# Optimization experiments

Measured on AMD Instinct MI355X. Metric: run time of the kernel, lower is better.

The kernel has to match this reference:

```python
import jax, jax.numpy as jnp
import numpy as np

B, FEAT, H, W = 16, 64, 32, 32


def setup_inputs() -> dict:
    key = jax.random.key(0)
    ks = jax.random.split(key, 8)
    s = 0.05
    return {
        "x": jax.random.normal(ks[0], (B, 2 * FEAT, H, W), jnp.float32),
        # i2s_conv: MaskConv(2F -> 4F, 1x1, maskB with group=1 == all-ones), bias=False
        "w_i2s": jax.random.normal(ks[1], (4 * FEAT, 2 * FEAT), jnp.float32) * s,
        # left/right state-to-state Conv2d(F -> 4F, kernel (2,1)), with bias
        "w_left": jax.random.normal(ks[2], (4 * FEAT, FEAT, 2), jnp.float32) * s,
        "b_left": jax.random.normal(ks[3], (4 * FEAT,), jnp.float32) * s,
        "w_right": jax.random.normal(ks[4], (4 * FEAT, FEAT, 2), jnp.float32) * s,
        "b_right": jax.random.normal(ks[5], (4 * FEAT,), jnp.float32) * s,
        # skip_conv: MaskConv(F -> 2F, 1x1, maskB group=1 == plain conv), bias=True
        "w_skip": jax.random.normal(ks[6], (2 * FEAT, FEAT), jnp.float32) * s,
        "b_skip": jax.random.normal(ks[7], (2 * FEAT,), jnp.float32) * s,
    }


def _shift_right_w(a):  # F.pad(a,(1,0,...))[..., :-1]
    return jnp.pad(a, ((0, 0), (0, 0), (0, 0), (1, 0)))[:, :, :, :-1]


def _shift_left_w(a):  # F.pad(a,(0,1,...))[..., 1:]
    return jnp.pad(a, ((0, 0), (0, 0), (0, 0), (0, 1)))[:, :, :, 1:]


def _shift_down_h(a):  # pad one row on top, drop last row
    return jnp.pad(a, ((0, 0), (0, 0), (1, 0), (0, 0)))[:, :, :-1, :]


def _s2s(hprev, w, b, wshift):
    # pad(top=1, side=1) + Conv2d kernel (2,1) + crop one column, expressed as
    # two 1x1 contractions on width-shifted / (width+height)-shifted maps.
    hw = wshift(hprev)            # [B,F,H,W] shifted one column
    hd = _shift_down_h(hw)        # additionally shifted one row down
    return (jnp.einsum('bchw,oc->bohw', hd, w[:, :, 0])
            + jnp.einsum('bchw,oc->bohw', hw, w[:, :, 1])
            + b[None, :, None, None])


def _forward(x, w_i2s, w_left, b_left, w_right, b_right, w_skip, b_skip):
    b_, c2, h_, w_ = x.shape
    f = c2 // 2
    hmap = jnp.einsum('bchw,oc->bohw', x, w_i2s)  # [B,4F,H,W]
    left_h = hmap   # stew: input-to-state shared between directions
    right_h = hmap
    zeros = jnp.zeros((b_, f, h_, w_), x.dtype)

    def step(carry, _):
        lc, lh, rc, rh = carry
        pre = jax.nn.sigmoid(_s2s(lh, w_left, b_left, _shift_right_w) + left_h)
        o, fg, ig, g = jnp.split(pre, 4, axis=1)
        lc = fg * lc + ig * g
        lh = o * jnp.tanh(lc)
        pre = jax.nn.sigmoid(_s2s(rh, w_right, b_right, _shift_left_w) + right_h)
        o, fg, ig, g = jnp.split(pre, 4, axis=1)
        rc = fg * rc + ig * g
        rh = o * jnp.tanh(rc)
        return (lc, lh, rc, rh), None

    (lc, lh, rc, rh), _ = jax.lax.scan(step, (zeros, zeros, zeros, zeros), None, length=h_)
    rh = _shift_down_h(rh)  # unstew + shift right stream down one row
    out_h = lh + rh         # [B,F,H,W]
    skip = jnp.einsum('bchw,oc->bohw', out_h, w_skip) + b_skip[None, :, None, None]
    return x + skip


def reference(x, w_i2s, w_left, b_left, w_right, b_right, w_skip, b_skip):
    return _forward(x, w_i2s, w_left, b_left, w_right, b_right, w_skip, b_skip)
```

## Files before the change

### kernel.cpp

```cpp
#include <hip/hip_runtime.h>


using bf16   = __bf16;
using bf16x8 = __attribute__((ext_vector_type(8))) __bf16;
using f32x4  = __attribute__((ext_vector_type(4))) float;

#define SCOPE_AGENT __HIP_MEMORY_SCOPE_AGENT
#define LOG2E 1.4426950408889634f
#define K2E   2.8853900817779268f

__device__ __forceinline__ bf16x8 bzero8() {
  bf16x8 v;
#pragma unroll
  for (int e = 0; e < 8; ++e) v[e] = (bf16)0.0f;
  return v;
}
__device__ __forceinline__ unsigned short f2bu(float f) {
  bf16 b = (bf16)f;
  return __builtin_bit_cast(unsigned short, b);
}
__device__ __forceinline__ float bu2f(unsigned short u) {
  return __uint_as_float(((unsigned)u) << 16);
}
__device__ __forceinline__ float dw_lo(unsigned u) { return __uint_as_float(u << 16); }
__device__ __forceinline__ float dw_hi(unsigned u) { return __uint_as_float(u & 0xffff0000u); }

__global__ void prep_kernel(const float* __restrict__ w_i2s,
                            const float* __restrict__ w_left,
                            const float* __restrict__ w_right,
                            const float* __restrict__ w_skip,
                            bf16* __restrict__ WnI, bf16* __restrict__ WnL,
                            bf16* __restrict__ WnR, bf16* __restrict__ WnS) {
  int t = blockIdx.x * 256 + threadIdx.x;
  if (t < 32768) {
    WnI[t] = (bf16)w_i2s[t];
    int o = t >> 7, k = t & 127;
    int src = (k < 64) ? (o * 128 + k * 2) : (o * 128 + (k - 64) * 2 + 1);
    WnL[t] = (bf16)(w_left[src] * LOG2E);
    WnR[t] = (bf16)(w_right[src] * LOG2E);
    if (t < 8192) WnS[t] = (bf16)w_skip[t];
  }
}

__global__ __launch_bounds__(256, 2)
void hmap_kernel(const float* __restrict__ x, const bf16* __restrict__ Wn,
                 const float* __restrict__ bL, const float* __restrict__ bR,
                 ushort4* __restrict__ hmapL, ushort4* __restrict__ hmapR) {
  __shared__ __align__(16) bf16 At[64 * 128];
  const int tile = blockIdx.x;
  const int b = tile >> 4, h0 = (tile & 15) << 1;
  const int t = threadIdx.x;
  const float* xb = x + (size_t)(b * 128) * 1024 + h0 * 32;
#pragma unroll
  for (int i = 0; i < 8; ++i) {
    int idx = t + 256 * i;
    int cc = idx >> 4, m4 = idx & 15;
    f32x4 v = *(const f32x4*)(xb + (size_t)cc * 1024 + m4 * 4);
#pragma unroll
    for (int e = 0; e < 4; ++e) {
      int m = m4 * 4 + e;
      int kb = (cc * 2) ^ ((m & 7) << 4);
      *(bf16*)((char*)At + m * 256 + kb) = (bf16)v[e];
    }
  }
  __syncthreads();
  const int wv = t >> 6, l = t & 63;
  const int l15 = l & 15, lq = l >> 4;
  const int c = wv * 16 + l15;
  bf16x8 bfrag[4][4];
#pragma unroll
  for (int g = 0; g < 4; ++g)
#pragma unroll
    for (int kk = 0; kk < 4; ++kk)
      bfrag[g][kk] = *(const bf16x8*)(Wn + (g * 64 + c) * 128 + kk * 32 + lq * 8);
  float blq[4], brq[4];
#pragma unroll
  for (int g = 0; g < 4; ++g) {
    blq[g] = bL[g * 64 + c] * LOG2E;
    brq[g] = bR[g * 64 + c] * LOG2E;
  }
  f32x4 acc[4][4];
  const f32x4 fz = {0.f, 0.f, 0.f, 0.f};
#pragma unroll
  for (int ms = 0; ms < 4; ++ms)
#pragma unroll
    for (int g = 0; g < 4; ++g) acc[ms][g] = fz;
#pragma unroll
  for (int kk = 0; kk < 4; ++kk) {
#pragma unroll
    for (int ms = 0; ms < 4; ++ms) {
      int m = ms * 16 + l15;
      int kb = ((kk * 32 + lq * 8) * 2) ^ ((m & 7) << 4);
      bf16x8 a = *(const bf16x8*)((const char*)At + m * 256 + kb);
#pragma unroll
      for (int g = 0; g < 4; ++g)
        acc[ms][g] =
            __builtin_amdgcn_mfma_f32_16x16x32_bf16(a, bfrag[g][kk], acc[ms][g], 0, 0, 0);
    }
  }
  const int pix0 = tile * 64;
#pragma unroll
  for (int ms = 0; ms < 4; ++ms)
#pragma unroll
    for (int j = 0; j < 4; ++j) {
      int p = pix0 + ms * 16 + lq * 4 + j;
      ushort4 hl, hr;
      float a0 = acc[ms][0][j] * LOG2E, a1 = acc[ms][1][j] * LOG2E;
      float a2 = acc[ms][2][j] * LOG2E, a3 = acc[ms][3][j] * LOG2E;
      hl.x = f2bu(a0 + blq[0]); hl.y = f2bu(a1 + blq[1]);
      hl.z = f2bu(a2 + blq[2]); hl.w = f2bu(a3 + blq[3]);
      hr.x = f2bu(a0 + brq[0]); hr.y = f2bu(a1 + brq[1]);
      hr.z = f2bu(a2 + brq[2]); hr.w = f2bu(a3 + brq[3]);
      hmapL[(size_t)p * 64 + c] = hl;
      hmapR[(size_t)p * 64 + c] = hr;
    }
}

__global__ __launch_bounds__(512, 4)
void scan_kernel(bf16* __restrict__ lhLout, bf16* __restrict__ lhRout,
                 const ushort4* __restrict__ hmapL,
                 const ushort4* __restrict__ hmapR,
                 const bf16* __restrict__ WnL, const bf16* __restrict__ WnR,
                 bf16* __restrict__ ring, unsigned* __restrict__ prodFlag,
                 unsigned* __restrict__ consFlag) {
  __shared__ __align__(16) bf16 buf[2][3 * 32 * 64];
  __shared__ __align__(16) ushort4 hlds[64 * 65];
  const int blk = blockIdx.x;
  const int q = blk & 31, tl = blk >> 5;
  const bool right = (q & 1) != 0;
  const int b = q >> 1;
  const int r0 = tl * 2;
  const int t = threadIdx.x;
  const int dw = right ? 1 : -1;
  bf16* __restrict__ lout = right ? lhRout : lhLout;
  const bf16* __restrict__ Wn = right ? WnR : WnL;
  const ushort4* __restrict__ hsrc =
      (right ? hmapR : hmapL) + (size_t)(b * 1024 + r0 * 32) * 64;
  const int w8 = t >> 6, l = t & 63, l15 = l & 15, lq = l >> 4;
  const int wv = w8 & 3, mhalf = w8 >> 2;
  const int c = wv * 16 + l15;
  const int wb_ = mhalf * 16;

#pragma unroll
  for (int i = 0; i < 8; ++i) {
    int idx = t + 512 * i;
    int px = idx >> 6, cc = idx & 63;
    hlds[px * 65 + cc] = hsrc[idx];
  }
#pragma unroll
  for (int i = 0; i < 2; ++i) {
    int idx = t + 512 * i;
    if (idx < 768) ((bf16x8*)buf[0])[idx] = bzero8();
  }
  if (t < 256) ((bf16x8*)buf[1])[t] = bzero8();

  bf16x8 bfrag[4][4];
#pragma unroll
  for (int g = 0; g < 4; ++g)
#pragma unroll
    for (int kk = 0; kk < 4; ++kk)
      bfrag[g][kk] = *(const bf16x8*)(Wn + (g * 64 + c) * 128 + kk * 32 + lq * 8);
  float lcA[4], lcB[4];
#pragma unroll
  for (int j = 0; j < 4; ++j) {
    lcA[j] = 0.0f;
    lcB[j] = 0.0f;
  }

  const unsigned* pBelow = prodFlag + (size_t)(blk - 32) * 32;
  const unsigned* cAbove = consFlag + (size_t)(blk + 32) * 32;
  unsigned* myProd = prodFlag + (size_t)blk * 32;
  unsigned* myCons = consFlag + (size_t)blk * 32;

  const int wsrc = wb_ + l15 + dw;
  const bool oob = (unsigned)wsrc >= 32u;
  const int wc = wsrc & 31;
  const int swz = (wc & 7) << 4;

  __syncthreads();

#pragma unroll 1
  for (int s = 0; s < 32; ++s) {
    bf16* curb = buf[s & 1];
    bf16* nxtb = buf[(s + 1) & 1];
    const bool consume = (tl > 0) && (s > 0);
    const bool publish = (tl < 15) && (s < 31);
    bf16* slotOut = ring + (size_t)(((s & 3) * 512) + blk) * 2048;

    if (consume) {
      const unsigned tgt = (unsigned)s;
      while (__hip_atomic_load(pBelow, __ATOMIC_RELAXED, SCOPE_AGENT) < tgt)
        __builtin_amdgcn_s_sleep(1);
      const bf16* slotIn =
          ring + (size_t)((((s - 1) & 3) * 512) + (blk - 32)) * 2048;
      int w = t >> 4, c4 = t & 15;
      const unsigned long long* src =
          (const unsigned long long*)(slotIn + w * 64 + c4 * 8);
      unsigned long long d0 = __hip_atomic_load(src, __ATOMIC_RELAXED, SCOPE_AGENT);
      int off = (w * 128 + c4 * 16) ^ ((w & 7) << 4);
      *(unsigned long long*)((char*)curb + off) = d0;
      int w2 = 0;
      (void)w2;
    }
    if (publish && s >= 4) {
      const unsigned tgt = (unsigned)(s - 3);
      while (__hip_atomic_load(cAbove, __ATOMIC_RELAXED, SCOPE_AGENT) < tgt)
        __builtin_amdgcn_s_sleep(1);
    }

    {
      f32x4 acc[4];
#pragma unroll
      for (int j2 = 0; j2 < 2; ++j2) {
        int w0 = wb_ + lq * 4 + j2 * 2;
        ushort4 h0 = hlds[(32 + w0) * 65 + c];
        ushort4 h1 = hlds[(32 + w0 + 1) * 65 + c];
        acc[0][j2 * 2] = bu2f(h0.x); acc[0][j2 * 2 + 1] = bu2f(h1.x);
        acc[1][j2 * 2] = bu2f(h0.y); acc[1][j2 * 2 + 1] = bu2f(h1.y);
        acc[2][j2 * 2] = bu2f(h0.z); acc[2][j2 * 2 + 1] = bu2f(h1.z);
        acc[3][j2 * 2] = bu2f(h0.w); acc[3][j2 * 2 + 1] = bu2f(h1.w);
      }
#pragma unroll
      for (int kk = 0; kk < 4; ++kk) {
        const int srcr = 1 + (kk >> 1);
        const int c0 = (kk & 1) * 32 + lq * 8;
        int aoff = ((srcr * 32 + wc) * 128 + c0 * 2) ^ swz;
        bf16x8 a = *(const bf16x8*)((const char*)curb + aoff);
        if (oob) a = bzero8();
#pragma unroll
        for (int g = 0; g < 4; ++g)
          acc[g] = __builtin_amdgcn_mfma_f32_16x16x32_bf16(a, bfrag[g][kk], acc[g], 0, 0, 0);
      }
#pragma unroll
      for (int j = 0; j < 4; ++j) {
        const int w = wb_ + lq * 4 + j;
        float e0 = __builtin_amdgcn_exp2f(-acc[0][j]);
        float e1 = __builtin_amdgcn_exp2f(-acc[1][j]);
        float e2 = __builtin_amdgcn_exp2f(-acc[2][j]);
        float e3 = __builtin_amdgcn_exp2f(-acc[3][j]);
        float fg = __builtin_amdgcn_rcpf(1.0f + e1);
        float igg = __builtin_amdgcn_rcpf((1.0f + e2) * (1.0f + e3));
        float lcv = fg * lcA[j] + K2E * igg;
        lcA[j] = lcv;
        float ey = __builtin_amdgcn_exp2f(-lcv);
        float lh = (1.0f - ey) * __builtin_amdgcn_rcpf((1.0f + e0) * (1.0f + ey));
        bf16 vb = (bf16)lh;
        int woff = ((2 * 32 + w) * 128 + c * 2) ^ ((w & 7) << 4);
        *(bf16*)((char*)nxtb + woff) = vb;
        if (publish) {
          unsigned u = (unsigned)__builtin_bit_cast(unsigned short, vb);
          unsigned pv = (unsigned)__shfl_xor((int)u, 1);
          if ((l & 1) == 0) {
            unsigned dword = u | (pv << 16);
            __hip_atomic_store((unsigned*)(slotOut + w * 64 + (c & ~1)), dword,
                               __ATOMIC_RELAXED, SCOPE_AGENT);
          }
        }
      }
    }
    __syncthreads();
    if (publish && t == 0)
      __hip_atomic_store(myProd, (unsigned)(s + 1), __ATOMIC_RELAXED, SCOPE_AGENT);
    if (consume && t == 64)
      __hip_atomic_store(myCons, (unsigned)s, __ATOMIC_RELAXED, SCOPE_AGENT);

    {
      f32x4 acc[4];
#pragma unroll
      for (int j2 = 0; j2 < 2; ++j2) {
        int w0 = wb_ + lq * 4 + j2 * 2;
        ushort4 h0 = hlds[w0 * 65 + c];
        ushort4 h1 = hlds[(w0 + 1) * 65 + c];
        acc[0][j2 * 2] = bu2f(h0.x); acc[0][j2 * 2 + 1] = bu2f(h1.x);
        acc[1][j2 * 2] = bu2f(h0.y); acc[1][j2 * 2 + 1] = bu2f(h1.y);
        acc[2][j2 * 2] = bu2f(h0.z); acc[2][j2 * 2 + 1] = bu2f(h1.z);
        acc[3][j2 * 2] = bu2f(h0.w); acc[3][j2 * 2 + 1] = bu2f(h1.w);
      }
#pragma unroll
      for (int kk = 0; kk < 4; ++kk) {
        const int srcr = kk >> 1;
        const int c0 = (kk & 1) * 32 + lq * 8;
        int aoff = ((srcr * 32 + wc) * 128 + c0 * 2) ^ swz;
        bf16x8 a = *(const bf16x8*)((const char*)curb + aoff);
        if (oob) a = bzero8();
#pragma unroll
        for (int g = 0; g < 4; ++g)
          acc[g] = __builtin_amdgcn_mfma_f32_16x16x32_bf16(a, bfrag[g][kk], acc[g], 0, 0, 0);
      }
#pragma unroll
      for (int j = 0; j < 4; ++j) {
        const int w = wb_ + lq * 4 + j;
        float e0 = __builtin_amdgcn_exp2f(-acc[0][j]);
        float e1 = __builtin_amdgcn_exp2f(-acc[1][j]);
        float e2 = __builtin_amdgcn_exp2f(-acc[2][j]);
        float e3 = __builtin_amdgcn_exp2f(-acc[3][j]);
        float fg = __builtin_amdgcn_rcpf(1.0f + e1);
        float igg = __builtin_amdgcn_rcpf((1.0f + e2) * (1.0f + e3));
        float lcv = fg * lcB[j] + K2E * igg;
        lcB[j] = lcv;
        float ey = __builtin_amdgcn_exp2f(-lcv);
        float lh = (1.0f - ey) * __builtin_amdgcn_rcpf((1.0f + e0) * (1.0f + ey));
        int woff = ((1 * 32 + w) * 128 + c * 2) ^ ((w & 7) << 4);
        *(bf16*)((char*)nxtb + woff) = (bf16)lh;
      }
    }
    __syncthreads();
  }

  {
    int R = 1 + (t >> 8), rem = t & 255;
    int w = rem >> 3, c8 = rem & 7;
    int off = ((R * 32 + w) * 128 + c8 * 16) ^ ((w & 7) << 4);
    bf16x8 v = *(const bf16x8*)((const char*)buf[0] + off);
    *(bf16x8*)(lout + (size_t)((b * 32 + r0 + R - 1) * 32 + w) * 64 + c8 * 8) = v;
  }
}

__global__ __launch_bounds__(256, 2)
void final_kernel(const float* __restrict__ x, const bf16* __restrict__ lhL,
                  const bf16* __restrict__ lhR, const bf16* __restrict__ Wn,
                  const float* __restrict__ b_skip, float* __restrict__ out) {
  __shared__ __align__(16) bf16 At[64 * 64];
  __shared__ __align__(16) float smemT[128 * 72];
  const int tile = blockIdx.x;
  const int b = tile >> 4, h0 = (tile & 15) << 1;
  const int t = threadIdx.x;
#pragma unroll
  for (int i = 0; i < 2; ++i) {
    int idx = t + 256 * i;
    int m = idx >> 3, c8 = idx & 7;
    int h = h0 + (m >> 5), w = m & 31;
    size_t p = (size_t)(b * 32 + h) * 32 + w;
    bf16x8 vL = *(const bf16x8*)(lhL + p * 64 + c8 * 8);
    bf16x8 v;
    if (h > 0) {
      bf16x8 vR = *(const bf16x8*)(lhR + (p - 32) * 64 + c8 * 8);
#pragma unroll
      for (int e = 0; e < 8; ++e) v[e] = (bf16)((float)vL[e] + (float)vR[e]);
    } else {
      v = vL;
    }
    int kb = (c8 * 16) ^ ((m & 7) << 4);
    *(bf16x8*)((char*)At + m * 128 + kb) = v;
  }
  __syncthreads();
  const int wv = t >> 6, l = t & 63;
  const int l15 = l & 15, lq = l >> 4;
  const int c = wv * 16 + l15;
  bf16x8 bfrag[2][2];
#pragma unroll
  for (int g = 0; g < 2; ++g)
#pragma unroll
    for (int kk = 0; kk < 2; ++kk)
      bfrag[g][kk] = *(const bf16x8*)(Wn + (g * 64 + c) * 64 + kk * 32 + lq * 8);
  f32x4 acc[4][2];
  const f32x4 fz = {0.f, 0.f, 0.f, 0.f};
#pragma unroll
  for (int ms = 0; ms < 4; ++ms)
#pragma unroll
    for (int g = 0; g < 2; ++g) acc[ms][g] = fz;
#pragma unroll
  for (int kk = 0; kk < 2; ++kk) {
#pragma unroll
    for (int ms = 0; ms < 4; ++ms) {
      int m = ms * 16 + l15;
      int kb = ((kk * 32 + lq * 8) * 2) ^ ((m & 7) << 4);
      bf16x8 a = *(const bf16x8*)((const char*)At + m * 128 + kb);
#pragma unroll
      for (int g = 0; g < 2; ++g)
        acc[ms][g] =
            __builtin_amdgcn_mfma_f32_16x16x32_bf16(a, bfrag[g][kk], acc[ms][g], 0, 0, 0);
    }
  }
  float bsk[2];
#pragma unroll
  for (int g = 0; g < 2; ++g) bsk[g] = b_skip[g * 64 + c];
#pragma unroll
  for (int ms = 0; ms < 4; ++ms)
#pragma unroll
    for (int g = 0; g < 2; ++g)
#pragma unroll
      for (int j = 0; j < 4; ++j) {
        int m = ms * 16 + lq * 4 + j;
        int n = g * 64 + c;
        smemT[n * 72 + m] = acc[ms][g][j] + bsk[g];
      }
  __syncthreads();
  const float* xb = x + (size_t)(b * 128) * 1024 + h0 * 32;
  float* ob = out + (size_t)(b * 128) * 1024 + h0 * 32;
#pragma unroll
  for (int i = 0; i < 8; ++i) {
    int idx = t + 256 * i;
    int o2 = idx >> 4, m4 = idx & 15;
    f32x4 s = *(const f32x4*)(&smemT[o2 * 72 + m4 * 4]);
    f32x4 xv = *(const f32x4*)(xb + (size_t)o2 * 1024 + m4 * 4);
#pragma unroll
    for (int e = 0; e < 4; ++e) s[e] += xv[e];
    *(f32x4*)(ob + (size_t)o2 * 1024 + m4 * 4) = s;
  }
}

extern "C" void kernel_launch(void* const* d_in, const int* in_sizes, int n_in,
                              void* d_out, int out_size, void* d_ws, size_t ws_size,
                              hipStream_t stream) {
  const float* x       = (const float*)d_in[0];
  const float* w_i2s   = (const float*)d_in[1];
  const float* w_left  = (const float*)d_in[2];
  const float* b_left  = (const float*)d_in[3];
  const float* w_right = (const float*)d_in[4];
  const float* b_right = (const float*)d_in[5];
  const float* w_skip  = (const float*)d_in[6];
  const float* b_skip  = (const float*)d_in[7];
  float* out = (float*)d_out;
  char* ws = (char*)d_ws;

  bf16*     lhL   = (bf16*)(ws + 0x0000000);
  bf16*     lhR   = (bf16*)(ws + 0x0200000);
  ushort4*  hmapL = (ushort4*)(ws + 0x0400000);
  ushort4*  hmapR = (ushort4*)(ws + 0x0C00000);
  bf16*     ring  = (bf16*)(ws + 0x1400000);
  unsigned* prodF = (unsigned*)(ws + 0x1C00000);
  unsigned* consF = (unsigned*)(ws + 0x1C10000);
  bf16*     WnI   = (bf16*)(ws + 0x1C20000);
  bf16*     WnL   = (bf16*)(ws + 0x1C30000);
  bf16*     WnR   = (bf16*)(ws + 0x1C40000);
  bf16*     WnS   = (bf16*)(ws + 0x1C50000);

  hipMemsetAsync(ws + 0x1C00000, 0, 0x20000, stream);
  prep_kernel<<<128, 256, 0, stream>>>(w_i2s, w_left, w_right, w_skip, WnI, WnL, WnR, WnS);
  hmap_kernel<<<256, 256, 0, stream>>>(x, WnI, b_left, b_right, hmapL, hmapR);
  scan_kernel<<<512, 512, 0, stream>>>(lhL, lhR, hmapL, hmapR, WnL, WnR,
                                       ring, prodF, consF);
  final_kernel<<<256, 256, 0, stream>>>(x, lhL, lhR, WnS, b_skip, out);
}
```

Before: 174.0 us.

## Feed ring halo rows straight into MFMA registers and drop mid-step barrier

The scan kernel no longer stages the halo row received from the block below into shared memory. Each lane now loads its MFMA A-fragments for that row directly from the global ring buffer into registers. This shrinks the LDS ping-pong buffer from three rows to two and removes one __syncthreads per step. The producer and consumer flag stores move to the end-of-step barrier, which may delay the publish signal to neighbouring blocks by half a step.

```diff
diff --git a/kernel.cpp b/kernel.cpp
--- a/kernel.cpp
+++ b/kernel.cpp
@@ -4,6 +4,7 @@
 using bf16   = __bf16;
 using bf16x8 = __attribute__((ext_vector_type(8))) __bf16;
 using f32x4  = __attribute__((ext_vector_type(4))) float;
+using u64x2  = __attribute__((ext_vector_type(2))) unsigned long long;
 
 #define SCOPE_AGENT __HIP_MEMORY_SCOPE_AGENT
 #define LOG2E 1.4426950408889634f
@@ -22,8 +23,6 @@
 __device__ __forceinline__ float bu2f(unsigned short u) {
   return __uint_as_float(((unsigned)u) << 16);
 }
-__device__ __forceinline__ float dw_lo(unsigned u) { return __uint_as_float(u << 16); }
-__device__ __forceinline__ float dw_hi(unsigned u) { return __uint_as_float(u & 0xffff0000u); }
 
 __global__ void prep_kernel(const float* __restrict__ w_i2s,
                             const float* __restrict__ w_left,
@@ -123,7 +122,7 @@
                  const bf16* __restrict__ WnL, const bf16* __restrict__ WnR,
                  bf16* __restrict__ ring, unsigned* __restrict__ prodFlag,
                  unsigned* __restrict__ consFlag) {
-  __shared__ __align__(16) bf16 buf[2][3 * 32 * 64];
+  __shared__ __align__(16) bf16 buf[2][2 * 32 * 64];
   __shared__ __align__(16) ushort4 hlds[64 * 65];
   const int blk = blockIdx.x;
   const int q = blk & 31, tl = blk >> 5;
@@ -147,12 +146,7 @@
     int px = idx >> 6, cc = idx & 63;
     hlds[px * 65 + cc] = hsrc[idx];
   }
-#pragma unroll
-  for (int i = 0; i < 2; ++i) {
-    int idx = t + 512 * i;
-    if (idx < 768) ((bf16x8*)buf[0])[idx] = bzero8();
-  }
-  if (t < 256) ((bf16x8*)buf[1])[t] = bzero8();
+  ((bf16x8*)buf[0])[t] = bzero8();
 
   bf16x8 bfrag[4][4];
 #pragma unroll
@@ -160,11 +154,11 @@
 #pragma unroll
     for (int kk = 0; kk < 4; ++kk)
       bfrag[g][kk] = *(const bf16x8*)(Wn + (g * 64 + c) * 128 + kk * 32 + lq * 8);
-  float lcA[4], lcB[4];
+  float lc0[4], lc1[4];
 #pragma unroll
   for (int j = 0; j < 4; ++j) {
-    lcA[j] = 0.0f;
-    lcB[j] = 0.0f;
+    lc0[j] = 0.0f;
+    lc1[j] = 0.0f;
   }
 
   const unsigned* pBelow = prodFlag + (size_t)(blk - 32) * 32;
@@ -187,20 +181,22 @@
     const bool publish = (tl < 15) && (s < 31);
     bf16* slotOut = ring + (size_t)(((s & 3) * 512) + blk) * 2048;
 
+    bf16x8 a_ring0 = bzero8(), a_ring1 = bzero8();
     if (consume) {
       const unsigned tgt = (unsigned)s;
       while (__hip_atomic_load(pBelow, __ATOMIC_RELAXED, SCOPE_AGENT) < tgt)
         __builtin_amdgcn_s_sleep(1);
-      const bf16* slotIn =
-          ring + (size_t)((((s - 1) & 3) * 512) + (blk - 32)) * 2048;
-      int w = t >> 4, c4 = t & 15;
-      const unsigned long long* src =
-          (const unsigned long long*)(slotIn + w * 64 + c4 * 8);
-      unsigned long long d0 = __hip_atomic_load(src, __ATOMIC_RELAXED, SCOPE_AGENT);
-      int off = (w * 128 + c4 * 16) ^ ((w & 7) << 4);
-      *(unsigned long long*)((char*)curb + off) = d0;
-      int w2 = 0;
-      (void)w2;
+      if (!oob) {
+        const unsigned long long* slotIn = (const unsigned long long*)(
+            ring + (size_t)((((s - 1) & 3) * 512) + (blk - 32)) * 2048 + wc * 64);
+        u64x2 v0, v1;
+        v0[0] = __hip_atomic_load(slotIn + lq * 2, __ATOMIC_RELAXED, SCOPE_AGENT);
+        v0[1] = __hip_atomic_load(slotIn + lq * 2 + 1, __ATOMIC_RELAXED, SCOPE_AGENT);
+        v1[0] = __hip_atomic_load(slotIn + 8 + lq * 2, __ATOMIC_RELAXED, SCOPE_AGENT);
+        v1[1] = __hip_atomic_load(slotIn + 8 + lq * 2 + 1, __ATOMIC_RELAXED, SCOPE_AGENT);
+        a_ring0 = __builtin_bit_cast(bf16x8, v0);
+        a_ring1 = __builtin_bit_cast(bf16x8, v1);
+      }
     }
     if (publish && s >= 4) {
       const unsigned tgt = (unsigned)(s - 3);
@@ -222,7 +218,7 @@
       }
 #pragma unroll
       for (int kk = 0; kk < 4; ++kk) {
-        const int srcr = 1 + (kk >> 1);
+        const int srcr = kk >> 1;
         const int c0 = (kk & 1) * 32 + lq * 8;
         int aoff = ((srcr * 32 + wc) * 128 + c0 * 2) ^ swz;
         bf16x8 a = *(const bf16x8*)((const char*)curb + aoff);
@@ -240,12 +236,12 @@
         float e3 = __builtin_amdgcn_exp2f(-acc[3][j]);
         float fg = __builtin_amdgcn_rcpf(1.0f + e1);
         float igg = __builtin_amdgcn_rcpf((1.0f + e2) * (1.0f + e3));
-        float lcv = fg * lcA[j] + K2E * igg;
-        lcA[j] = lcv;
+        float lcv = fg * lc1[j] + K2E * igg;
+        lc1[j] = lcv;
         float ey = __builtin_amdgcn_exp2f(-lcv);
         float lh = (1.0f - ey) * __builtin_amdgcn_rcpf((1.0f + e0) * (1.0f + ey));
         bf16 vb = (bf16)lh;
-        int woff = ((2 * 32 + w) * 128 + c * 2) ^ ((w & 7) << 4);
+        int woff = ((1 * 32 + w) * 128 + c * 2) ^ ((w & 7) << 4);
         *(bf16*)((char*)nxtb + woff) = vb;
         if (publish) {
           unsigned u = (unsigned)__builtin_bit_cast(unsigned short, vb);
@@ -258,11 +254,6 @@
         }
       }
     }
-    __syncthreads();
-    if (publish && t == 0)
-      __hip_atomic_store(myProd, (unsigned)(s + 1), __ATOMIC_RELAXED, SCOPE_AGENT);
-    if (consume && t == 64)
-      __hip_atomic_store(myCons, (unsigned)s, __ATOMIC_RELAXED, SCOPE_AGENT);
 
     {
       f32x4 acc[4];
@@ -277,10 +268,15 @@
         acc[3][j2 * 2] = bu2f(h0.w); acc[3][j2 * 2 + 1] = bu2f(h1.w);
       }
 #pragma unroll
-      for (int kk = 0; kk < 4; ++kk) {
-        const int srcr = kk >> 1;
+      for (int g = 0; g < 4; ++g)
+        acc[g] = __builtin_amdgcn_mfma_f32_16x16x32_bf16(a_ring0, bfrag[g][0], acc[g], 0, 0, 0);
+#pragma unroll
+      for (int g = 0; g < 4; ++g)
+        acc[g] = __builtin_amdgcn_mfma_f32_16x16x32_bf16(a_ring1, bfrag[g][1], acc[g], 0, 0, 0);
+#pragma unroll
+      for (int kk = 2; kk < 4; ++kk) {
         const int c0 = (kk & 1) * 32 + lq * 8;
-        int aoff = ((srcr * 32 + wc) * 128 + c0 * 2) ^ swz;
+        int aoff = ((0 * 32 + wc) * 128 + c0 * 2) ^ swz;
         bf16x8 a = *(const bf16x8*)((const char*)curb + aoff);
         if (oob) a = bzero8();
 #pragma unroll
@@ -296,23 +292,28 @@
         float e3 = __builtin_amdgcn_exp2f(-acc[3][j]);
         float fg = __builtin_amdgcn_rcpf(1.0f + e1);
         float igg = __builtin_amdgcn_rcpf((1.0f + e2) * (1.0f + e3));
-        float lcv = fg * lcB[j] + K2E * igg;
-        lcB[j] = lcv;
+        float lcv = fg * lc0[j] + K2E * igg;
+        lc0[j] = lcv;
         float ey = __builtin_amdgcn_exp2f(-lcv);
         float lh = (1.0f - ey) * __builtin_amdgcn_rcpf((1.0f + e0) * (1.0f + ey));
-        int woff = ((1 * 32 + w) * 128 + c * 2) ^ ((w & 7) << 4);
+        int woff = ((0 * 32 + w) * 128 + c * 2) ^ ((w & 7) << 4);
         *(bf16*)((char*)nxtb + woff) = (bf16)lh;
       }
     }
+
     __syncthreads();
+    if (publish && t == 0)
+      __hip_atomic_store(myProd, (unsigned)(s + 1), __ATOMIC_RELAXED, SCOPE_AGENT);
+    if (consume && t == 64)
+      __hip_atomic_store(myCons, (unsigned)s, __ATOMIC_RELAXED, SCOPE_AGENT);
   }
 
   {
-    int R = 1 + (t >> 8), rem = t & 255;
+    int row = t >> 8, rem = t & 255;
     int w = rem >> 3, c8 = rem & 7;
-    int off = ((R * 32 + w) * 128 + c8 * 16) ^ ((w & 7) << 4);
+    int off = ((row * 32 + w) * 128 + c8 * 16) ^ ((w & 7) << 4);
     bf16x8 v = *(const bf16x8*)((const char*)buf[0] + off);
-    *(bf16x8*)(lout + (size_t)((b * 32 + r0 + R - 1) * 32 + w) * 64 + c8 * 8) = v;
+    *(bf16x8*)(lout + (size_t)((b * 32 + r0 + row) * 32 + w) * 64 + c8 * 8) = v;
   }
 }
 
```

Result: slower. 205.1 us (+17.9%).
